# Optimization experiments

Measured on AMD Instinct MI355X. Metric: run time of the kernel, lower is better.

Reference implementation:

```python
import jax, jax.numpy as jnp
import numpy as np

NEG_SLOPE = 0.2  # PyG GATConv default


def _gat_layer(x, src, dst, W, a_s, a_d, b, num_nodes):
    H, C = a_s.shape
    h = (x @ W).reshape(num_nodes, H, C)                     # [N,H,C]
    alpha_src = jnp.einsum('nhc,hc->nh', h, a_s)             # [N,H]
    alpha_dst = jnp.einsum('nhc,hc->nh', h, a_d)             # [N,H]
    e = jax.nn.leaky_relu(alpha_src[src] + alpha_dst[dst], NEG_SLOPE)  # [E,H]
    # segment softmax over incoming edges of each destination node
    m = jax.lax.stop_gradient(jax.ops.segment_max(e, dst, num_segments=num_nodes))
    e = jnp.exp(e - m[dst])
    den = jax.ops.segment_sum(e, dst, num_segments=num_nodes)
    alpha = e / den[dst]                                     # [E,H]
    msg = h[src] * alpha[:, :, None]                         # [E,H,C]
    out = jax.ops.segment_sum(msg, dst, num_segments=num_nodes)
    return out.reshape(num_nodes, H * C) + b


def setup_inputs() -> dict:
    key = jax.random.key(0)
    ks = jax.random.split(key, 10)
    N, E, D, H, C = 100000, 1600000, 128, 4, 32
    s = 1.0 / np.sqrt(D)
    return {
        'x': jax.random.normal(ks[0], (N, D), jnp.float32),
        'edge_index': jax.random.randint(ks[1], (2, E), 0, N, jnp.int64),
        'W1': jax.random.normal(ks[2], (D, H * C), jnp.float32) * s,
        'a_src1': jax.random.normal(ks[3], (H, C), jnp.float32) * s,
        'a_dst1': jax.random.normal(ks[4], (H, C), jnp.float32) * s,
        'b1': jnp.zeros((H * C,), jnp.float32),
        'W2': jax.random.normal(ks[5], (H * C, H * C), jnp.float32) * s,
        'a_src2': jax.random.normal(ks[6], (H, C), jnp.float32) * s,
        'a_dst2': jax.random.normal(ks[7], (H, C), jnp.float32) * s,
        'b2': jnp.zeros((H * C,), jnp.float32),
    }


def reference(x, edge_index, W1, a_src1, a_dst1, b1, W2, a_src2, a_dst2, b2):
    N = x.shape[0]
    loop = jnp.arange(N, dtype=edge_index.dtype)  # PyG add_self_loops=True
    src = jnp.concatenate([edge_index[0], loop])
    dst = jnp.concatenate([edge_index[1], loop])
    h = _gat_layer(x, src, dst, W1, a_src1, a_dst1, b1, N)
    h = jax.nn.relu(h)
    h = _gat_layer(h, src, dst, W2, a_src2, a_dst2, b2, N)
    return jax.nn.relu(h)
```

## Files before the change

kernel.cpp:

```cpp
#include <hip/hip_runtime.h>
#include <cstdint>
#include <cstddef>

#define NEG_SLOPE 0.2f
#define BIN_SHIFT 9
#define BCAP 16384
#define LOG2E 1.4426950408889634f

typedef short bf16x8 __attribute__((ext_vector_type(8)));
typedef float f32x4 __attribute__((ext_vector_type(4)));

#if __has_builtin(__builtin_amdgcn_exp2f)
#define EXP2(x) __builtin_amdgcn_exp2f(x)
#else
#define EXP2(x) exp2f(x)
#endif

static __device__ __forceinline__ unsigned short bf16r(float f) {
    unsigned u = __float_as_uint(f);
    return (unsigned short)((u + 0x7fffu + ((u >> 16) & 1u)) >> 16);
}
static __device__ __forceinline__ float bfu_lo(unsigned u) { return __uint_as_float(u << 16); }
static __device__ __forceinline__ float bfu_hi(unsigned u) { return __uint_as_float(u & 0xffff0000u); }

__global__ __launch_bounds__(256) void wprep_k(const float* __restrict__ W1, const float* __restrict__ W2,
                                               unsigned short* __restrict__ Wh1, unsigned short* __restrict__ Wl1,
                                               unsigned short* __restrict__ Wh2, unsigned short* __restrict__ Wl2,
                                               int* __restrict__ bcnt) {
    if (blockIdx.x == 0) bcnt[threadIdx.x] = 0;
    int t = blockIdx.x * 256 + threadIdx.x;
    const float* W;
    unsigned short *Wh, *Wl;
    int idx;
    if (t < 16384) { W = W1; Wh = Wh1; Wl = Wl1; idx = t; }
    else           { W = W2; Wh = Wh2; Wl = Wl2; idx = t - 16384; }
    int c = idx >> 7;
    int k = idx & 127;
    float w = W[(size_t)k * 128 + c];
    unsigned short h = bf16r(w);
    float lo = w - __uint_as_float((unsigned)h << 16);
    int dst = (k >> 5) * 4096 + (c >> 4) * 512 + (((k >> 3) & 3) * 16 + (c & 15)) * 8 + (k & 7);
    Wh[dst] = h;
    Wl[dst] = bf16r(lo);
}

__global__ __launch_bounds__(256) void bin_k(const int* __restrict__ srcI, const int* __restrict__ dstI,
                                             int E, int N, int K, int* __restrict__ bcnt,
                                             int* __restrict__ tmpE) {
    __shared__ int hist[256];
    __shared__ int lbase[256];
    __shared__ int lstart[256];
    __shared__ int cur[256];
    __shared__ int sc[256];
    __shared__ int staged[4096];
    __shared__ unsigned char bs[4096];
    const int t = threadIdx.x;
    const int M = E + N;
    const int chunk0 = blockIdx.x * 4096;
    hist[t] = 0;
    __syncthreads();

    int pk[16], bk[16];
#pragma unroll
    for (int jj = 0; jj < 4; ++jj) {
        int ebase = chunk0 + (t + jj * 256) * 4;
        if (ebase + 4 <= E) {
            int4 s4 = *(const int4*)&srcI[ebase];
            int4 d4 = *(const int4*)&dstI[ebase];
            int ssv[4] = {s4.x, s4.y, s4.z, s4.w};
            int ddv[4] = {d4.x, d4.y, d4.z, d4.w};
#pragma unroll
            for (int j = 0; j < 4; ++j) {
                int q = jj * 4 + j;
                bk[q] = -1;
                if ((unsigned)ddv[j] < (unsigned)N && (unsigned)ssv[j] < (unsigned)N) {
                    bk[q] = ddv[j] >> BIN_SHIFT;
                    pk[q] = (ssv[j] << 9) | (ddv[j] & 511);
                    atomicAdd(&hist[bk[q]], 1);
                }
            }
        } else {
#pragma unroll
            for (int j = 0; j < 4; ++j) {
                int q = jj * 4 + j;
                int i = ebase + j;
                bk[q] = -1;
                if (i < M) {
                    int ss, dd;
                    if (i < E) { ss = srcI[i]; dd = dstI[i]; }
                    else       { ss = i - E;  dd = ss; }
                    if ((unsigned)dd < (unsigned)N && (unsigned)ss < (unsigned)N) {
                        bk[q] = dd >> BIN_SHIFT;
                        pk[q] = (ss << 9) | (dd & 511);
                        atomicAdd(&hist[bk[q]], 1);
                    }
                }
            }
        }
    }
    __syncthreads();
    const int h = hist[t];
    lbase[t] = (h > 0) ? atomicAdd(&bcnt[t], h) : 0;
    sc[t] = h;
    __syncthreads();
    for (int off = 1; off < 256; off <<= 1) {
        int v = (t >= off) ? sc[t - off] : 0;
        __syncthreads();
        sc[t] += v;
        __syncthreads();
    }
    lstart[t] = sc[t] - h;
    cur[t]    = sc[t] - h;
    __syncthreads();
#pragma unroll
    for (int j = 0; j < 16; ++j) {
        if (bk[j] >= 0) {
            int r = atomicAdd(&cur[bk[j]], 1);
            staged[r] = pk[j];
            bs[r] = (unsigned char)bk[j];
        }
    }
    const int total = sc[255];
    __syncthreads();
    for (int s = t; s < total; s += 256) {
        int b = bs[s];
        int posInBucket = lbase[b] + (s - lstart[b]);
        if (posInBucket < BCAP) tmpE[(size_t)b * BCAP + posInBucket] = staged[s];
    }
}

__global__ __launch_bounds__(256) void scatter_csr_k(const int* __restrict__ tmpE,
                                                     const int* __restrict__ bcnt,
                                                     int* __restrict__ rowptr,
                                                     int* __restrict__ colOff,
                                                     int N, int K) {
    __shared__ int pre[256];
    __shared__ int cur[512];
    __shared__ int ss[256];
    const int t = threadIdx.x;
    const int b = blockIdx.x;

    int bc = (t < K) ? min(bcnt[t], BCAP) : 0;
    pre[t] = bc;
    __syncthreads();
    for (int off = 1; off < 256; off <<= 1) {
        int v = (t >= off) ? pre[t - off] : 0;
        __syncthreads();
        pre[t] += v;
        __syncthreads();
    }
    const int base_b = (b == 0) ? 0 : pre[b - 1];
    const int cnt_b  = pre[b] - base_b;
    if (b == K - 1 && t == 0) rowptr[N] = pre[K - 1];

    const int nlo = b << BIN_SHIFT;
    const int nhi = min(nlo + (1 << BIN_SHIFT), N);
    const int nn  = nhi - nlo;
    const int* te = tmpE + (size_t)b * BCAP;

    cur[t] = 0;
    cur[t + 256] = 0;
    __syncthreads();
    for (int i0 = t * 4; i0 < cnt_b; i0 += 1024) {
        int4 v = *(const int4*)&te[i0];
        int vv[4] = {v.x, v.y, v.z, v.w};
#pragma unroll
        for (int j = 0; j < 4; ++j)
            if (i0 + j < cnt_b) atomicAdd(&cur[vv[j] & 511], 1);
    }
    __syncthreads();

    int v0 = cur[2 * t], v1 = cur[2 * t + 1];
    ss[t] = v0 + v1;
    __syncthreads();
    for (int off = 1; off < 256; off <<= 1) {
        int v = (t >= off) ? ss[t - off] : 0;
        __syncthreads();
        ss[t] += v;
        __syncthreads();
    }
    int e0 = (t == 0) ? 0 : ss[t - 1];
    int e1 = e0 + v0;
    if (2 * t < nn)     rowptr[nlo + 2 * t]     = base_b + e0;
    if (2 * t + 1 < nn) rowptr[nlo + 2 * t + 1] = base_b + e1;
    cur[2 * t] = e0;
    cur[2 * t + 1] = e1;
    __syncthreads();

    for (int i0 = t * 4; i0 < cnt_b; i0 += 1024) {
        int4 v = *(const int4*)&te[i0];
        int vv[4] = {v.x, v.y, v.z, v.w};
#pragma unroll
        for (int j = 0; j < 4; ++j) {
            if (i0 + j < cnt_b) {
                int r = atomicAdd(&cur[vv[j] & 511], 1);
                colOff[base_b + r] = ((unsigned)vv[j] >> 9) << 8;
            }
        }
    }
}

__global__ __launch_bounds__(256) void gemm_mfma_k(const float* __restrict__ X,
                                                   const unsigned short* __restrict__ Wh,
                                                   const unsigned short* __restrict__ Wl,
                                                   const float* __restrict__ a_s,
                                                   const float* __restrict__ a_d,
                                                   unsigned short* __restrict__ Hout,
                                                   float* __restrict__ asrc,
                                                   float* __restrict__ adst,
                                                   int N) {
    __shared__ __align__(16) unsigned short hstage[4][32][132];
    const int tid = threadIdx.x;
    const int wid = tid >> 6;
    const int l   = tid & 63;
    const int l15 = l & 15;
    const int lh  = l >> 4;
    const int waveRow = blockIdx.x * 128 + wid * 32;
    if (waveRow >= N) return;

    f32x4 acc[2][8];
#pragma unroll
    for (int m = 0; m < 2; ++m)
#pragma unroll
        for (int f = 0; f < 8; ++f)
#pragma unroll
            for (int c = 0; c < 4; ++c) acc[m][f][c] = 0.f;

    const int r0 = waveRow + l15;
    const int r1 = waveRow + 16 + l15;
    const size_t xoff0 = (size_t)min(r0, N - 1) * 128;
    const size_t xoff1 = (size_t)min(r1, N - 1) * 128;
    const int kb = lh * 8;

#pragma unroll
    for (int ks = 0; ks < 4; ++ks) {
        bf16x8 ah[2], al[2];
#pragma unroll
        for (int m = 0; m < 2; ++m) {
            const float* xp = X + (m ? xoff1 : xoff0) + ks * 32 + kb;
            float4 v0 = *(const float4*)xp;
            float4 v1 = *(const float4*)(xp + 4);
            float xs[8] = {v0.x, v0.y, v0.z, v0.w, v1.x, v1.y, v1.z, v1.w};
#pragma unroll
            for (int j = 0; j < 8; ++j) {
                unsigned short h = bf16r(xs[j]);
                float hf = __uint_as_float((unsigned)h << 16);
                ah[m][j] = (short)h;
                al[m][j] = (short)bf16r(xs[j] - hf);
            }
        }
        const unsigned short* wbh = Wh + ks * 4096 + l * 8;
        const unsigned short* wbl = Wl + ks * 4096 + l * 8;
#pragma unroll
        for (int f = 0; f < 8; ++f) {
            bf16x8 wh = *(const bf16x8*)(wbh + f * 512);
            bf16x8 wl = *(const bf16x8*)(wbl + f * 512);
#pragma unroll
            for (int m = 0; m < 2; ++m) {
                acc[m][f] = __builtin_amdgcn_mfma_f32_16x16x32_bf16(ah[m], wh, acc[m][f], 0, 0, 0);
                acc[m][f] = __builtin_amdgcn_mfma_f32_16x16x32_bf16(al[m], wh, acc[m][f], 0, 0, 0);
                acc[m][f] = __builtin_amdgcn_mfma_f32_16x16x32_bf16(ah[m], wl, acc[m][f], 0, 0, 0);
            }
        }
    }

    float asf[8], adf[8];
#pragma unroll
    for (int f = 0; f < 8; ++f) {
        asf[f] = a_s[f * 16 + l15];
        adf[f] = a_d[f * 16 + l15];
    }
    const int q = l15;
#pragma unroll
    for (int m = 0; m < 2; ++m) {
#pragma unroll
        for (int r = 0; r < 4; ++r) {
            float ps[4] = {0.f, 0.f, 0.f, 0.f};
            float pd[4] = {0.f, 0.f, 0.f, 0.f};
#pragma unroll
            for (int f = 0; f < 8; ++f) {
                float v = acc[m][f][r];
                ps[f >> 1] = fmaf(v, asf[f], ps[f >> 1]);
                pd[f >> 1] = fmaf(v, adf[f], pd[f >> 1]);
                hstage[wid][m * 16 + lh * 4 + r][f * 16 + l15] = bf16r(v);
            }
#pragma unroll
            for (int mask = 1; mask < 16; mask <<= 1) {
#pragma unroll
                for (int h = 0; h < 4; ++h) {
                    ps[h] += __shfl_xor(ps[h], mask);
                    pd[h] += __shfl_xor(pd[h], mask);
                }
            }
            int row = waveRow + m * 16 + lh * 4 + r;
            if (q < 8 && row < N) {
                float v0 = (q & 1) ? ps[1] : ps[0];
                float v1 = (q & 1) ? ps[3] : ps[2];
                float vs = (q & 2) ? v1 : v0;
                float w0 = (q & 1) ? pd[1] : pd[0];
                float w1 = (q & 1) ? pd[3] : pd[2];
                float vd = (q & 2) ? w1 : w0;
                if (q < 4) asrc[row * 4 + q] = vs * LOG2E;
                else       adst[row * 4 + (q - 4)] = vd * LOG2E;
            }
        }
    }

#pragma unroll
    for (int it = 0; it < 8; ++it) {
        int row = it * 4 + lh;
        const unsigned short* hp = &hstage[wid][row][l15 * 8];
        uint2 aa = *(const uint2*)hp;
        uint2 bb = *(const uint2*)(hp + 4);
        int grow = waveRow + row;
        if (grow < N) {
            uint4 o;
            o.x = aa.x; o.y = aa.y; o.z = bb.x; o.w = bb.y;
            *(uint4*)&Hout[(size_t)grow * 128 + l15 * 8] = o;
        }
    }
}

__global__ __launch_bounds__(256) void aggregate_k(const unsigned short* __restrict__ Hbuf,
                                                   const float* __restrict__ asrc,
                                                   const float* __restrict__ adst,
                                                   const int* __restrict__ rowptr,
                                                   const int* __restrict__ colOff,
                                                   const float* __restrict__ bias,
                                                   float* __restrict__ out, int N) {
    int wave = (blockIdx.x * 256 + threadIdx.x) >> 6;
    int lane = threadIdx.x & 63;
    if (wave >= N) return;
    const int n = wave;
    const int c0 = lane * 2;
    const int head = c0 >> 5;
    const float adh = adst[n * 4 + head];
    const char* Hb = (const char*)Hbuf;
    const char* As = (const char*)asrc;
    const int hoff = c0 * 2;
    const int aoff = head * 4;

    int b = __builtin_amdgcn_readfirstlane(rowptr[n]);
    int e = __builtin_amdgcn_readfirstlane(rowptr[n + 1]);
    float acc0 = 0.f, acc1 = 0.f, sw = 0.f;
    for (int p = b; p < e; p += 8) {
        int off[8];
#pragma unroll
        for (int j = 0; j < 8; ++j) off[j] = colOff[min(p + j, e - 1)];
        float a[8];
#pragma unroll
        for (int j = 0; j < 8; ++j) a[j] = *(const float*)(As + (off[j] >> 4) + aoff);
        unsigned hu[8];
#pragma unroll
        for (int j = 0; j < 8; ++j) hu[j] = *(const unsigned*)(Hb + off[j] + hoff);
#pragma unroll
        for (int j = 0; j < 8; ++j) {
            float x = a[j] + adh;
            float w = (p + j < e) ? EXP2(fmaxf(x, NEG_SLOPE * x)) : 0.f;
            sw += w;
            acc0 = fmaf(w, bfu_lo(hu[j]), acc0);
            acc1 = fmaf(w, bfu_hi(hu[j]), acc1);
        }
    }
    float inv = 1.f / sw;
    float o0 = fmaxf(acc0 * inv + bias[c0], 0.f);
    float o1 = fmaxf(acc1 * inv + bias[c0 + 1], 0.f);
    *(float2*)&out[(size_t)n * 128 + c0] = make_float2(o0, o1);
}


extern "C" void kernel_launch(void* const* d_in, const int* in_sizes, int n_in,
                              void* d_out, int out_size, void* d_ws, size_t ws_size,
                              hipStream_t stream) {
    const float* X   = (const float*)d_in[0];
    const int*   EI  = (const int*)d_in[1];
    const float* W1  = (const float*)d_in[2];
    const float* as1 = (const float*)d_in[3];
    const float* ad1 = (const float*)d_in[4];
    const float* b1  = (const float*)d_in[5];
    const float* W2  = (const float*)d_in[6];
    const float* as2 = (const float*)d_in[7];
    const float* ad2 = (const float*)d_in[8];
    const float* b2  = (const float*)d_in[9];

    const int N = in_sizes[0] / 128;
    const int E = in_sizes[1] / 2;
    const int M = E + N;
    const int K = (N + (1 << BIN_SHIFT) - 1) >> BIN_SHIFT;
    const int* srcI = EI;
    const int* dstI = EI + E;

    char* w = (char*)d_ws;
    auto alloc = [&](size_t bytes) {
        char* p = w;
        w += (bytes + 255) & ~(size_t)255;
        return p;
    };
    unsigned short* Hbuf = (unsigned short*)alloc((size_t)N * 128 * 2);
    float* asrc   = (float*)alloc((size_t)N * 4 * 4);
    float* adst   = (float*)alloc((size_t)N * 4 * 4);
    int*   rowptr = (int*)alloc((size_t)(N + 1) * 4);
    int*   colOff = (int*)alloc((size_t)M * 4);
    int*   tmpE   = (int*)alloc((size_t)K * BCAP * 4);
    int*   bcnt   = (int*)alloc(256 * 4);
    unsigned short* Wt1h = (unsigned short*)alloc(128 * 128 * 2);
    unsigned short* Wt1l = (unsigned short*)alloc(128 * 128 * 2);
    unsigned short* Wt2h = (unsigned short*)alloc(128 * 128 * 2);
    unsigned short* Wt2l = (unsigned short*)alloc(128 * 128 * 2);

    const int gemmBlocks = (N + 127) / 128;
    float* out = (float*)d_out;

    wprep_k<<<128, 256, 0, stream>>>(W1, W2, Wt1h, Wt1l, Wt2h, Wt2l, bcnt);
    bin_k<<<(M + 4095) / 4096, 256, 0, stream>>>(srcI, dstI, E, N, K, bcnt, tmpE);
    scatter_csr_k<<<K, 256, 0, stream>>>(tmpE, bcnt, rowptr, colOff, N, K);
    gemm_mfma_k<<<gemmBlocks, 256, 0, stream>>>(X, Wt1h, Wt1l, as1, ad1, Hbuf, asrc, adst, N);
    aggregate_k<<<((size_t)N * 64 + 255) / 256, 256, 0, stream>>>(Hbuf, asrc, adst, rowptr, colOff, b1, out, N);
    gemm_mfma_k<<<gemmBlocks, 256, 0, stream>>>(out, Wt2h, Wt2l, as2, ad2, Hbuf, asrc, adst, N);
    aggregate_k<<<((size_t)N * 64 + 255) / 256, 256, 0, stream>>>(Hbuf, asrc, adst, rowptr, colOff, b2, out, N);
}
```

Measured before the change: 367.9 us.

## Use finer 128-node bins and drop LDS staging in edge binning

Shrinks the CSR-build bin width from 512 to 128 destination nodes, so there are up to 1024 buckets (782 for this graph) instead of 196. The LDS staging pass and per-block prefix scan in the binning kernel are removed, and edges are written straight to global buckets using per-block bucket bases plus a local atomic counter. Scatter blocks now handle smaller buckets with a 128-entry histogram and the bucket prefix is computed over 1024 entries. Gains are fewer barriers and more parallelism in the scatter stage; the risk is less coalesced global writes in binning and BCAP=4096 overflowing on skewed degree distributions.

```diff
diff --git a/kernel.cpp b/kernel.cpp
--- a/kernel.cpp
+++ b/kernel.cpp
@@ -3,8 +3,8 @@
 #include <cstddef>
 
 #define NEG_SLOPE 0.2f
-#define BIN_SHIFT 9
-#define BCAP 16384
+#define BIN_SHIFT 7
+#define BCAP 4096
 #define LOG2E 1.4426950408889634f
 
 typedef short bf16x8 __attribute__((ext_vector_type(8)));
@@ -27,7 +27,7 @@
                                                unsigned short* __restrict__ Wh1, unsigned short* __restrict__ Wl1,
                                                unsigned short* __restrict__ Wh2, unsigned short* __restrict__ Wl2,
                                                int* __restrict__ bcnt) {
-    if (blockIdx.x == 0) bcnt[threadIdx.x] = 0;
+    if (blockIdx.x < 4) bcnt[blockIdx.x * 256 + threadIdx.x] = 0;
     int t = blockIdx.x * 256 + threadIdx.x;
     const float* W;
     unsigned short *Wh, *Wl;
@@ -47,17 +47,13 @@
 __global__ __launch_bounds__(256) void bin_k(const int* __restrict__ srcI, const int* __restrict__ dstI,
                                              int E, int N, int K, int* __restrict__ bcnt,
                                              int* __restrict__ tmpE) {
-    __shared__ int hist[256];
-    __shared__ int lbase[256];
-    __shared__ int lstart[256];
-    __shared__ int cur[256];
-    __shared__ int sc[256];
-    __shared__ int staged[4096];
-    __shared__ unsigned char bs[4096];
+    __shared__ int hist[1024];
+    __shared__ int lbase[1024];
     const int t = threadIdx.x;
     const int M = E + N;
     const int chunk0 = blockIdx.x * 4096;
-    hist[t] = 0;
+#pragma unroll
+    for (int j = 0; j < 4; ++j) hist[t + j * 256] = 0;
     __syncthreads();
 
     int pk[16], bk[16];
@@ -75,7 +71,7 @@
                 bk[q] = -1;
                 if ((unsigned)ddv[j] < (unsigned)N && (unsigned)ssv[j] < (unsigned)N) {
                     bk[q] = ddv[j] >> BIN_SHIFT;
-                    pk[q] = (ssv[j] << 9) | (ddv[j] & 511);
+                    pk[q] = (ssv[j] << BIN_SHIFT) | (ddv[j] & 127);
                     atomicAdd(&hist[bk[q]], 1);
                 }
             }
@@ -91,7 +87,7 @@
                     else       { ss = i - E;  dd = ss; }
                     if ((unsigned)dd < (unsigned)N && (unsigned)ss < (unsigned)N) {
                         bk[q] = dd >> BIN_SHIFT;
-                        pk[q] = (ss << 9) | (dd & 511);
+                        pk[q] = (ss << BIN_SHIFT) | (dd & 127);
                         atomicAdd(&hist[bk[q]], 1);
                     }
                 }
@@ -99,33 +95,23 @@
         }
     }
     __syncthreads();
-    const int h = hist[t];
-    lbase[t] = (h > 0) ? atomicAdd(&bcnt[t], h) : 0;
-    sc[t] = h;
-    __syncthreads();
-    for (int off = 1; off < 256; off <<= 1) {
-        int v = (t >= off) ? sc[t - off] : 0;
-        __syncthreads();
-        sc[t] += v;
-        __syncthreads();
-    }
-    lstart[t] = sc[t] - h;
-    cur[t]    = sc[t] - h;
+#pragma unroll
+    for (int j = 0; j < 4; ++j) {
+        int b = t + j * 256;
+        if (b < K) {
+            int h = hist[b];
+            lbase[b] = (h > 0) ? atomicAdd(&bcnt[b], h) : 0;
+            hist[b] = 0;
+        }
+    }
     __syncthreads();
 #pragma unroll
     for (int j = 0; j < 16; ++j) {
         if (bk[j] >= 0) {
-            int r = atomicAdd(&cur[bk[j]], 1);
-            staged[r] = pk[j];
-            bs[r] = (unsigned char)bk[j];
-        }
-    }
-    const int total = sc[255];
-    __syncthreads();
-    for (int s = t; s < total; s += 256) {
-        int b = bs[s];
-        int posInBucket = lbase[b] + (s - lstart[b]);
-        if (posInBucket < BCAP) tmpE[(size_t)b * BCAP + posInBucket] = staged[s];
+            int r = atomicAdd(&hist[bk[j]], 1);
+            int pos = lbase[bk[j]] + r;
+            if (pos < BCAP) tmpE[(size_t)bk[j] * BCAP + pos] = pk[j];
+        }
     }
 }
 
@@ -134,67 +120,79 @@
                                                      int* __restrict__ rowptr,
                                                      int* __restrict__ colOff,
                                                      int N, int K) {
-    __shared__ int pre[256];
-    __shared__ int cur[512];
-    __shared__ int ss[256];
+    __shared__ int tl[256];
+    __shared__ int allB[1025];
+    __shared__ int cur[128];
+    __shared__ int sc[128];
     const int t = threadIdx.x;
     const int b = blockIdx.x;
 
-    int bc = (t < K) ? min(bcnt[t], BCAP) : 0;
-    pre[t] = bc;
+    int v[4];
+    int run = 0;
+#pragma unroll
+    for (int j = 0; j < 4; ++j) {
+        int idx = 4 * t + j;
+        int x = (idx < K) ? min(bcnt[idx], BCAP) : 0;
+        v[j] = run;
+        run += x;
+    }
+    tl[t] = run;
     __syncthreads();
     for (int off = 1; off < 256; off <<= 1) {
-        int v = (t >= off) ? pre[t - off] : 0;
+        int u = (t >= off) ? tl[t - off] : 0;
         __syncthreads();
-        pre[t] += v;
+        tl[t] += u;
         __syncthreads();
     }
-    const int base_b = (b == 0) ? 0 : pre[b - 1];
-    const int cnt_b  = pre[b] - base_b;
-    if (b == K - 1 && t == 0) rowptr[N] = pre[K - 1];
+    int excl = (t == 0) ? 0 : tl[t - 1];
+#pragma unroll
+    for (int j = 0; j < 4; ++j) allB[4 * t + j] = excl + v[j];
+    if (t == 255) allB[1024] = tl[255];
+    __syncthreads();
+
+    const int base_b = allB[b];
+    const int cnt_b  = allB[b + 1] - base_b;
+    if (b == K - 1 && t == 0) rowptr[N] = allB[K];
 
     const int nlo = b << BIN_SHIFT;
     const int nhi = min(nlo + (1 << BIN_SHIFT), N);
     const int nn  = nhi - nlo;
     const int* te = tmpE + (size_t)b * BCAP;
 
-    cur[t] = 0;
-    cur[t + 256] = 0;
+    if (t < 128) cur[t] = 0;
     __syncthreads();
     for (int i0 = t * 4; i0 < cnt_b; i0 += 1024) {
-        int4 v = *(const int4*)&te[i0];
-        int vv[4] = {v.x, v.y, v.z, v.w};
+        int4 vv = *(const int4*)&te[i0];
+        int a[4] = {vv.x, vv.y, vv.z, vv.w};
 #pragma unroll
         for (int j = 0; j < 4; ++j)
-            if (i0 + j < cnt_b) atomicAdd(&cur[vv[j] & 511], 1);
-    }
-    __syncthreads();
-
-    int v0 = cur[2 * t], v1 = cur[2 * t + 1];
-    ss[t] = v0 + v1;
-    __syncthreads();
-    for (int off = 1; off < 256; off <<= 1) {
-        int v = (t >= off) ? ss[t - off] : 0;
+            if (i0 + j < cnt_b) atomicAdd(&cur[a[j] & 127], 1);
+    }
+    __syncthreads();
+
+    if (t < 128) sc[t] = cur[t];
+    __syncthreads();
+    for (int off = 1; off < 128; off <<= 1) {
+        int u = (t >= off && t < 128) ? sc[t - off] : 0;
         __syncthreads();
-        ss[t] += v;
+        if (t < 128) sc[t] += u;
         __syncthreads();
     }
-    int e0 = (t == 0) ? 0 : ss[t - 1];
-    int e1 = e0 + v0;
-    if (2 * t < nn)     rowptr[nlo + 2 * t]     = base_b + e0;
-    if (2 * t + 1 < nn) rowptr[nlo + 2 * t + 1] = base_b + e1;
-    cur[2 * t] = e0;
-    cur[2 * t + 1] = e1;
+    if (t < 128) {
+        int e0 = (t == 0) ? 0 : sc[t - 1];
+        if (t < nn) rowptr[nlo + t] = base_b + e0;
+        cur[t] = e0;
+    }
     __syncthreads();
 
     for (int i0 = t * 4; i0 < cnt_b; i0 += 1024) {
-        int4 v = *(const int4*)&te[i0];
-        int vv[4] = {v.x, v.y, v.z, v.w};
+        int4 vv = *(const int4*)&te[i0];
+        int a[4] = {vv.x, vv.y, vv.z, vv.w};
 #pragma unroll
         for (int j = 0; j < 4; ++j) {
             if (i0 + j < cnt_b) {
-                int r = atomicAdd(&cur[vv[j] & 511], 1);
-                colOff[base_b + r] = ((unsigned)vv[j] >> 9) << 8;
+                int r = atomicAdd(&cur[a[j] & 127], 1);
+                colOff[base_b + r] = ((unsigned)a[j] >> BIN_SHIFT) << 8;
             }
         }
     }
@@ -402,7 +400,7 @@
     int*   rowptr = (int*)alloc((size_t)(N + 1) * 4);
     int*   colOff = (int*)alloc((size_t)M * 4);
     int*   tmpE   = (int*)alloc((size_t)K * BCAP * 4);
-    int*   bcnt   = (int*)alloc(256 * 4);
+    int*   bcnt   = (int*)alloc(1024 * 4);
     unsigned short* Wt1h = (unsigned short*)alloc(128 * 128 * 2);
     unsigned short* Wt1l = (unsigned short*)alloc(128 * 128 * 2);
     unsigned short* Wt2h = (unsigned short*)alloc(128 * 128 * 2);
```

After: 368.4 us. Within noise of the previous version (+0.1%).
